# Kernel tuning notes

Measured on AMD Instinct MI355X. Metric: run time of the kernel, lower is better.

Reference implementation:

```python
import jax, jax.numpy as jnp
import numpy as np
import math

B, S, E = 2, 2048, 1024
H = 16                      # n_state_heads
STATE_SIZE = 16384
O = math.isqrt(STATE_SIZE // H)   # state_head_order = 32
C = E // (O * H)            # embedding_state_head_order_chunk_size = 2
N_BLOCKS = 12
EPS = 1e-5


def layernorm(x, g):
    mu = jnp.mean(x, axis=-1, keepdims=True)
    var = jnp.mean(jnp.square(x - mu), axis=-1, keepdims=True)
    return (x - mu) * jax.lax.rsqrt(var + EPS) * g


def setup_inputs() -> dict:
    key = jax.random.key(0)
    ks = jax.random.split(key, 8)
    return {
        "activations": jax.random.normal(ks[0], (B, S, E), dtype=jnp.float32),
        # note: torch init zeros W_up; we use small random weights so the scan is non-trivial
        "W_up": jax.random.normal(ks[1], (O, C), dtype=jnp.float32) * 0.02,
        "W_down": jax.random.normal(ks[2], (C, O), dtype=jnp.float32) * (0.02 * math.sqrt(STATE_SIZE)),
        "W_mru": jax.random.normal(ks[3], (E, E), dtype=jnp.float32) * (0.02 / math.sqrt(N_BLOCKS)),
        "g_ln1": jnp.ones((E,), dtype=jnp.float32),
        "g_ln2": jnp.ones((E,), dtype=jnp.float32),
        "W_mlp1": jax.random.normal(ks[4], (4 * E, E), dtype=jnp.float32) * 0.02,
        "W_mlp2": jax.random.normal(ks[5], (E, 4 * E), dtype=jnp.float32) * (0.02 / math.sqrt(N_BLOCKS)),
    }


def reference(activations, W_up, W_down, W_mru, g_ln1, g_ln2, W_mlp1, W_mlp2):
    x = activations                                   # [B,S,E]
    h = layernorm(x, g_ln1)
    hh = h.reshape(B, S, H, O, C)                     # unflatten(-1, (H, O, C))
    # state_matrices_up (Linear C->O, no bias) + eye  -> per-token transition matrices
    M = jnp.einsum('bshoc,qc->bshoq', hh, W_up) + jnp.eye(O, dtype=h.dtype)  # [B,S,H,O,O]
    Mt = jnp.swapaxes(M, 1, 2)                        # [B,H,S,O,O]
    # cumulative non-commutative matrix products along the sequence (log-depth scan)
    P = jax.lax.associative_scan(jnp.matmul, Mt, axis=2)  # P[t] = M_0 @ ... @ M_t
    states = jnp.swapaxes(P, 1, 2)                    # [B,S,H,O,O]
    # state_matrices_down (Linear O->C, no bias), then flatten(-3,-1)
    down = jnp.einsum('bshoq,cq->bshoc', states, W_down).reshape(B, S, E)
    mru_out = down @ W_mru.T
    x = x + mru_out
    y = layernorm(x, g_ln2)
    m = jax.nn.gelu(y @ W_mlp1.T, approximate=False) @ W_mlp2.T
    x = x + m
    new_state = states[-1]                            # faithful to torch states[-1] (last batch element): [S,H,O,O]
    return (x, new_state)
```

## Files before the change

### kernel.cpp

```cpp
#include <hip/hip_runtime.h>
#include <hip/hip_bf16.h>
#include <math.h>

#define Bb 2
#define Ss 2048
#define Ee 1024
#define Hh 16
#define Oo 32
#define Cc 2
#define EPSf 1e-5f
#define NSEG 64
#define SEGL 32
#define NGRP 8
#define GRPL 8

typedef __hip_bfloat16 bf16;
typedef __attribute__((ext_vector_type(8))) short short8;
typedef __attribute__((ext_vector_type(4))) float f32x4;

template <typename OT>
__global__ __launch_bounds__(256) void ln_kernel(const float* __restrict__ x,
                                                 const float* __restrict__ g,
                                                 OT* __restrict__ out) {
    __shared__ float red[8];
    int row = blockIdx.x;
    const float4* xr = (const float4*)(x + (size_t)row * Ee);
    float4 v = xr[threadIdx.x];
    float s = v.x + v.y + v.z + v.w;
#pragma unroll
    for (int off = 32; off > 0; off >>= 1) s += __shfl_xor(s, off);
    int wave = threadIdx.x >> 6, lane = threadIdx.x & 63;
    if (!lane) red[wave] = s;
    __syncthreads();
    float mu = (red[0] + red[1] + red[2] + red[3]) * (1.0f / Ee);
    float dx = v.x - mu, dy = v.y - mu, dz = v.z - mu, dw = v.w - mu;
    float sq = dx * dx + dy * dy + dz * dz + dw * dw;
#pragma unroll
    for (int off = 32; off > 0; off >>= 1) sq += __shfl_xor(sq, off);
    if (!lane) red[wave + 4] = sq;
    __syncthreads();
    float var = (red[4] + red[5] + red[6] + red[7]) * (1.0f / Ee);
    float rs = rsqrtf(var + EPSf);
    float4 gv = ((const float4*)g)[threadIdx.x];
    float o0 = dx * rs * gv.x, o1 = dy * rs * gv.y, o2 = dz * rs * gv.z, o3 = dw * rs * gv.w;
    if constexpr (sizeof(OT) == 4) {
        ((float4*)((float*)out + (size_t)row * Ee))[threadIdx.x] = make_float4(o0, o1, o2, o3);
    } else {
        __align__(8) bf16 t[4] = {__float2bfloat16(o0), __float2bfloat16(o1),
                                  __float2bfloat16(o2), __float2bfloat16(o3)};
        ((ushort4*)((unsigned short*)out + (size_t)row * Ee))[threadIdx.x] = *(const ushort4*)t;
    }
}

__device__ __forceinline__ void cvt4(const float* in, bf16* out, int i) {
    float4 v = ((const float4*)in)[i];
    __align__(8) bf16 t[4] = {__float2bfloat16(v.x), __float2bfloat16(v.y),
                              __float2bfloat16(v.z), __float2bfloat16(v.w)};
    ((ushort4*)out)[i] = *(const ushort4*)t;
}

__global__ __launch_bounds__(256) void f2bf3_kernel(const float* __restrict__ a, bf16* __restrict__ oa,
                                                    const float* __restrict__ b, bf16* __restrict__ ob,
                                                    const float* __restrict__ c, bf16* __restrict__ oc) {
    const int nA = (1024 * 1024) / 4;
    const int nB = (4 * 1024 * 1024) / 4;
    int i = blockIdx.x * 256 + threadIdx.x;
    if (i < nA) cvt4(a, oa, i);
    else if (i < nA + nB) cvt4(b, ob, i - nA);
    else cvt4(c, oc, i - nA - nB);
}

__device__ __forceinline__ void row_matmul(float e[32], const float* __restrict__ T) {
    float r[32];
#pragma unroll
    for (int q = 0; q < 32; ++q) r[q] = 0.f;
#pragma unroll
    for (int kk = 0; kk < 32; ++kk) {
        float ekk = e[kk];
        const float4* tr = (const float4*)(T + kk * 32);
#pragma unroll
        for (int j = 0; j < 8; ++j) {
            float4 tv = tr[j];
            r[4 * j + 0] = fmaf(ekk, tv.x, r[4 * j + 0]);
            r[4 * j + 1] = fmaf(ekk, tv.y, r[4 * j + 1]);
            r[4 * j + 2] = fmaf(ekk, tv.z, r[4 * j + 2]);
            r[4 * j + 3] = fmaf(ekk, tv.w, r[4 * j + 3]);
        }
    }
#pragma unroll
    for (int q = 0; q < 32; ++q) e[q] = r[q];
}

__global__ __launch_bounds__(256, 2) void scan_pass1(const float* __restrict__ h,
                                                     const float* __restrict__ Wup,
                                                     float* __restrict__ Ttot) {
    int wv = __builtin_amdgcn_readfirstlane((int)(threadIdx.x >> 6));
    int lane = threadIdx.x & 63;
    int o = lane & 31;
    int seg = blockIdx.x * 4 + wv;
    int chain = seg >> 6;
    int g = seg & 63;
    int b = chain >> 4, head = chain & 15;

    float wq[64];
#pragma unroll
    for (int j = 0; j < 16; ++j) ((float4*)wq)[j] = ((const float4*)Wup)[j];
    float p[32];
#pragma unroll
    for (int q = 0; q < 32; ++q) p[q] = (q == o) ? 1.0f : 0.0f;

    const float* hb = h + ((size_t)b * Ss + (size_t)g * SEGL) * Ee + head * 64;
    float4 ac[16];
#pragma unroll
    for (int j = 0; j < 16; ++j) ac[j] = ((const float4*)hb)[j];

    for (int st = 0; st < SEGL; ++st) {
        float4 an[16];
        if (st + 1 < SEGL) {
            const float4* hn = (const float4*)(hb + (size_t)(st + 1) * Ee);
#pragma unroll
            for (int j = 0; j < 16; ++j) an[j] = hn[j];
        }
        float s0 = 0.f, s1 = 0.f, u0 = 0.f, u1 = 0.f;
#pragma unroll
        for (int q = 0; q < 32; q += 2) {
            float4 v = ac[q >> 1];
            s0 = fmaf(p[q], v.x, s0);
            u0 = fmaf(p[q], v.y, u0);
            s1 = fmaf(p[q + 1], v.z, s1);
            u1 = fmaf(p[q + 1], v.w, u1);
        }
        float y0 = s0 + s1, y1 = u0 + u1;
#pragma unroll
        for (int q = 0; q < 32; ++q) p[q] = fmaf(y0, wq[2 * q], fmaf(y1, wq[2 * q + 1], p[q]));
        if (st + 1 < SEGL) {
#pragma unroll
            for (int j = 0; j < 16; ++j) ac[j] = an[j];
        }
    }
    if (lane < 32) {
        float* tb = Ttot + ((size_t)chain * NSEG + g) * 1024 + o * 32;
#pragma unroll
        for (int j = 0; j < 8; ++j)
            ((float4*)tb)[j] = make_float4(p[4 * j], p[4 * j + 1], p[4 * j + 2], p[4 * j + 3]);
    }
}

__global__ __launch_bounds__(64) void scan_pass2a(const float* __restrict__ Ttot,
                                                  float* __restrict__ Eexc,
                                                  float* __restrict__ Utot) {
    int lane = threadIdx.x & 63;
    int o = lane & 31;
    int grp = blockIdx.x;
    int chain = grp >> 3, k = grp & 7;
    float e[32];
#pragma unroll
    for (int q = 0; q < 32; ++q) e[q] = (q == o) ? 1.0f : 0.0f;
    for (int i = 0; i < GRPL; ++i) {
        int g = k * GRPL + i;
        if (lane < 32) {
            float* eb = Eexc + ((size_t)chain * NSEG + g) * 1024 + o * 32;
#pragma unroll
            for (int j = 0; j < 8; ++j)
                ((float4*)eb)[j] = make_float4(e[4 * j], e[4 * j + 1], e[4 * j + 2], e[4 * j + 3]);
        }
        row_matmul(e, Ttot + ((size_t)chain * NSEG + g) * 1024);
    }
    if (lane < 32) {
        float* ub = Utot + ((size_t)chain * NGRP + k) * 1024 + o * 32;
#pragma unroll
        for (int j = 0; j < 8; ++j)
            ((float4*)ub)[j] = make_float4(e[4 * j], e[4 * j + 1], e[4 * j + 2], e[4 * j + 3]);
    }
}

__global__ __launch_bounds__(64) void scan_pass2b(const float* __restrict__ Utot,
                                                  float* __restrict__ Wkp) {
    int lane = threadIdx.x & 63;
    int o = lane & 31;
    int chain = blockIdx.x;
    float w[32];
#pragma unroll
    for (int q = 0; q < 32; ++q) w[q] = (q == o) ? 1.0f : 0.0f;
    for (int k = 0; k < NGRP; ++k) {
        if (lane < 32) {
            float* wb = Wkp + ((size_t)chain * NGRP + k) * 1024 + o * 32;
#pragma unroll
            for (int j = 0; j < 8; ++j)
                ((float4*)wb)[j] = make_float4(w[4 * j], w[4 * j + 1], w[4 * j + 2], w[4 * j + 3]);
        }
        row_matmul(w, Utot + ((size_t)chain * NGRP + k) * 1024);
    }
}

__global__ __launch_bounds__(256, 2) void scan_pass3(const float* __restrict__ h,
                                                     const float* __restrict__ Wup,
                                                     const float* __restrict__ Wdn,
                                                     const float* __restrict__ Eexc,
                                                     const float* __restrict__ Wkp,
                                                     bf16* __restrict__ down,
                                                     float* __restrict__ state_out) {
    int wv = __builtin_amdgcn_readfirstlane((int)(threadIdx.x >> 6));
    int lane = threadIdx.x & 63;
    int o = lane & 31;
    int seg = blockIdx.x * 4 + wv;
    int chain = seg >> 6;
    int g = seg & 63;
    int b = chain >> 4, head = chain & 15;
    int k = g >> 3;

    float wq[64];
#pragma unroll
    for (int j = 0; j < 16; ++j) ((float4*)wq)[j] = ((const float4*)Wup)[j];
    float wd[64];
#pragma unroll
    for (int j = 0; j < 16; ++j) ((float4*)wd)[j] = ((const float4*)Wdn)[j];

    float G00 = 0.f, G01 = 0.f, G10 = 0.f, G11 = 0.f;
#pragma unroll
    for (int q = 0; q < 32; ++q) {
        G00 = fmaf(wq[2 * q + 0], wd[q], G00);
        G01 = fmaf(wq[2 * q + 0], wd[32 + q], G01);
        G10 = fmaf(wq[2 * q + 1], wd[q], G10);
        G11 = fmaf(wq[2 * q + 1], wd[32 + q], G11);
    }

    float wrow[32];
    const float* wb = Wkp + ((size_t)chain * NGRP + k) * 1024 + o * 32;
#pragma unroll
    for (int j = 0; j < 8; ++j) ((float4*)wrow)[j] = ((const float4*)wb)[j];
    const float* Eb = Eexc + ((size_t)chain * NSEG + g) * 1024;
    float p[32];
#pragma unroll
    for (int q = 0; q < 32; ++q) p[q] = 0.f;
#pragma unroll
    for (int kk = 0; kk < 32; ++kk) {
        float wkk = wrow[kk];
        const float4* er = (const float4*)(Eb + kk * 32);
#pragma unroll
        for (int j = 0; j < 8; ++j) {
            float4 ev = er[j];
            p[4 * j + 0] = fmaf(wkk, ev.x, p[4 * j + 0]);
            p[4 * j + 1] = fmaf(wkk, ev.y, p[4 * j + 1]);
            p[4 * j + 2] = fmaf(wkk, ev.z, p[4 * j + 2]);
            p[4 * j + 3] = fmaf(wkk, ev.w, p[4 * j + 3]);
        }
    }

    float d0 = 0.f, d1 = 0.f;
#pragma unroll
    for (int q = 0; q < 32; ++q) {
        d0 = fmaf(p[q], wd[q], d0);
        d1 = fmaf(p[q], wd[32 + q], d1);
    }

    const float* hb = h + ((size_t)b * Ss + (size_t)g * SEGL) * Ee + head * 64;
    bf16* db = down + ((size_t)b * Ss + (size_t)g * SEGL) * Ee + head * 64 + o * 2;
    float* sb = state_out + ((size_t)g * SEGL * Hh + head) * 1024 + o * 32;

    float4 ac[16];
#pragma unroll
    for (int j = 0; j < 16; ++j) ac[j] = ((const float4*)hb)[j];

    for (int st = 0; st < SEGL; ++st) {
        float4 an[16];
        if (st + 1 < SEGL) {
            const float4* hn = (const float4*)(hb + (size_t)(st + 1) * Ee);
#pragma unroll
            for (int j = 0; j < 16; ++j) an[j] = hn[j];
        }
        float s0 = 0.f, s1 = 0.f, u0 = 0.f, u1 = 0.f;
#pragma unroll
        for (int q = 0; q < 32; q += 2) {
            float4 v = ac[q >> 1];
            s0 = fmaf(p[q], v.x, s0);
            u0 = fmaf(p[q], v.y, u0);
            s1 = fmaf(p[q + 1], v.z, s1);
            u1 = fmaf(p[q + 1], v.w, u1);
        }
        float y0 = s0 + s1, y1 = u0 + u1;
#pragma unroll
        for (int q = 0; q < 32; ++q) p[q] = fmaf(y0, wq[2 * q], fmaf(y1, wq[2 * q + 1], p[q]));
        d0 = fmaf(y0, G00, fmaf(y1, G10, d0));
        d1 = fmaf(y0, G01, fmaf(y1, G11, d1));
        if (lane < 32) {
            __hip_bfloat162 dv;
            dv.x = __float2bfloat16(d0);
            dv.y = __float2bfloat16(d1);
            *(__hip_bfloat162*)(db + (size_t)st * Ee) = dv;
            if (b == Bb - 1) {
                float* sp = sb + (size_t)st * (Hh * 1024);
#pragma unroll
                for (int j = 0; j < 8; ++j)
                    ((float4*)sp)[j] = make_float4(p[4 * j], p[4 * j + 1], p[4 * j + 2], p[4 * j + 3]);
            }
        }
        if (st + 1 < SEGL) {
#pragma unroll
            for (int j = 0; j < 16; ++j) ac[j] = an[j];
        }
    }
}

__device__ __forceinline__ void load_lds16(const bf16* g, short* l) {
    __builtin_amdgcn_global_load_lds((const __attribute__((address_space(1))) unsigned int*)g,
                                     (__attribute__((address_space(3))) unsigned int*)l,
                                     16, 0, 0);
}


template <bool GELU, bool RESID, bool BF16OUT>
__global__ __launch_bounds__(256, 2) void mgemm64(const bf16* __restrict__ A,
                                                  const bf16* __restrict__ Wt,
                                                  const float* __restrict__ res,
                                                  float* __restrict__ Cf,
                                                  bf16* __restrict__ Cb,
                                                  int M, int N, int K) {
    __shared__ __align__(16) short As[3][64 * 32];
    __shared__ __align__(16) short Bs[3][128 * 32];
    int tid = threadIdx.x;
    int w = __builtin_amdgcn_readfirstlane(tid >> 6);
    int l = tid & 63;

    int nbm = M >> 6, nbn = N >> 7;
    int nwg = nbm * nbn;
    int cpx = nwg >> 3;
    int v = ((int)blockIdx.x & 7) * cpx + ((int)blockIdx.x >> 3);
    int sq = v >> 6, rem = v & 63;
    int sqPerRow = nbn >> 3;
    int bm = (sq / sqPerRow) * 8 + (rem >> 3);
    int bn = (sq % sqPerRow) * 8 + (rem & 7);

    int wr = w >> 1, wc = w & 1;
    int lr = l & 15;
    int lks = (((l >> 4) ^ ((lr >> 1) & 3)) * 8);

    int srow = tid >> 2;
    int scol = ((tid & 3) ^ ((tid >> 3) & 3)) * 8;
    const bf16* ga  = A + (size_t)(bm * 64 + srow) * K + scol;
    const bf16* gb0 = Wt + (size_t)(bn * 128 + srow) * K + scol;
    const bf16* gb1 = Wt + (size_t)(bn * 128 + 64 + srow) * K + scol;

    f32x4 acc[2][4];
#pragma unroll
    for (int m = 0; m < 2; ++m)
#pragma unroll
        for (int n = 0; n < 4; ++n) acc[m][n] = (f32x4){0.f, 0.f, 0.f, 0.f};

#define STAGE64(d, kt)                                       \
    do {                                                     \
        int _off = (kt) * 32;                                \
        load_lds16(ga + _off, &As[d][w * 512]);              \
        load_lds16(gb0 + _off, &Bs[d][w * 512]);             \
        load_lds16(gb1 + _off, &Bs[d][2048 + w * 512]);      \
    } while (0)

    const int NK = K >> 5;
    STAGE64(0, 0);
    STAGE64(1, 1);
    STAGE64(2, 2);
    asm volatile("s_waitcnt vmcnt(6)" ::: "memory");
    __builtin_amdgcn_sched_barrier(0);
    __builtin_amdgcn_s_barrier();

    for (int t = 0; t < NK; ++t) {
        int d = t % 3;
        short8 af[2], bfr[4];
#pragma unroll
        for (int m = 0; m < 2; ++m)
            af[m] = *(const short8*)&As[d][(wr * 32 + m * 16 + lr) * 32 + lks];
#pragma unroll
        for (int n = 0; n < 4; ++n)
            bfr[n] = *(const short8*)&Bs[d][(wc * 64 + n * 16 + lr) * 32 + lks];
        asm volatile("s_waitcnt lgkmcnt(0)" ::: "memory");
        __builtin_amdgcn_sched_barrier(0);
        __builtin_amdgcn_s_barrier();
        if (t + 3 < NK) STAGE64(d, t + 3);
        __builtin_amdgcn_sched_barrier(0);
        __builtin_amdgcn_s_setprio(1);
#pragma unroll
        for (int m = 0; m < 2; ++m)
#pragma unroll
            for (int n = 0; n < 4; ++n)
                acc[m][n] = __builtin_amdgcn_mfma_f32_16x16x32_bf16(af[m], bfr[n], acc[m][n], 0, 0, 0);
        __builtin_amdgcn_s_setprio(0);
        if (t + 3 < NK) {
            asm volatile("s_waitcnt vmcnt(6)" ::: "memory");
        } else if (t + 2 < NK) {
            asm volatile("s_waitcnt vmcnt(3)" ::: "memory");
        } else if (t + 1 < NK) {
            asm volatile("s_waitcnt vmcnt(0)" ::: "memory");
        }
        __builtin_amdgcn_sched_barrier(0);
        __builtin_amdgcn_s_barrier();
    }
#undef STAGE64

#pragma unroll
    for (int m = 0; m < 2; ++m) {
#pragma unroll
        for (int n = 0; n < 4; ++n) {
            int gr0 = bm * 64 + wr * 32 + m * 16 + (l >> 4) * 4;
            int gc = bn * 128 + wc * 64 + n * 16 + lr;
#pragma unroll
            for (int j = 0; j < 4; ++j) {
                float v2 = acc[m][n][j];
                if (GELU) v2 = 0.5f * v2 * (1.0f + erff(v2 * 0.70710678118654752f));
                if (RESID) v2 += res[(size_t)(gr0 + j) * N + gc];
                if (BF16OUT) Cb[(size_t)(gr0 + j) * N + gc] = __float2bfloat16(v2);
                else Cf[(size_t)(gr0 + j) * N + gc] = v2;
            }
        }
    }
}

__global__ __launch_bounds__(512, 2) void mgemm8(const bf16* __restrict__ A,
                                                 const bf16* __restrict__ Wt,
                                                 bf16* __restrict__ Cb,
                                                 int M, int N, int K) {
    __shared__ __align__(16) short As[3][256 * 32];
    __shared__ __align__(16) short Bs[3][256 * 32];
    int tid = threadIdx.x;
    int w = __builtin_amdgcn_readfirstlane(tid >> 6);
    int l = tid & 63;

    int nbm = M >> 8, nbn = N >> 8;
    int nwg = nbm * nbn;
    int cpx = nwg >> 3;
    int v = ((int)blockIdx.x & 7) * cpx + ((int)blockIdx.x >> 3);
    int sq = v >> 6, rem = v & 63;
    int sqPerRow = nbn >> 3;
    int bm = (sq / sqPerRow) * 8 + (rem >> 3);
    int bn = (sq % sqPerRow) * 8 + (rem & 7);

    int wr = w >> 2, wc = w & 3;
    int lr = l & 15;
    int lks = (((l >> 4) ^ ((lr >> 1) & 3)) * 8);

    int srow = tid >> 2;
    int scol = ((tid & 3) ^ ((tid >> 3) & 3)) * 8;
    const bf16* ga0 = A + (size_t)(bm * 256 + srow) * K + scol;
    const bf16* ga1 = A + (size_t)(bm * 256 + 128 + srow) * K + scol;
    const bf16* gb0 = Wt + (size_t)(bn * 256 + srow) * K + scol;
    const bf16* gb1 = Wt + (size_t)(bn * 256 + 128 + srow) * K + scol;

    f32x4 acc[8][4];
#pragma unroll
    for (int m = 0; m < 8; ++m)
#pragma unroll
        for (int n = 0; n < 4; ++n) acc[m][n] = (f32x4){0.f, 0.f, 0.f, 0.f};

#define STAGE8(d, kt)                                        \
    do {                                                     \
        int _off = (kt) * 32;                                \
        load_lds16(ga0 + _off, &As[d][w * 512]);             \
        load_lds16(ga1 + _off, &As[d][4096 + w * 512]);      \
        load_lds16(gb0 + _off, &Bs[d][w * 512]);             \
        load_lds16(gb1 + _off, &Bs[d][4096 + w * 512]);      \
    } while (0)

    const int NK = K >> 5;
    STAGE8(0, 0);
    STAGE8(1, 1);
    STAGE8(2, 2);
    asm volatile("s_waitcnt vmcnt(8)" ::: "memory");
    __builtin_amdgcn_sched_barrier(0);
    __builtin_amdgcn_s_barrier();

    for (int t = 0; t < NK; ++t) {
        int d = t % 3;
        short8 af[8], bfr[4];
#pragma unroll
        for (int m = 0; m < 8; ++m)
            af[m] = *(const short8*)&As[d][(wr * 128 + m * 16 + lr) * 32 + lks];
#pragma unroll
        for (int n = 0; n < 4; ++n)
            bfr[n] = *(const short8*)&Bs[d][(wc * 64 + n * 16 + lr) * 32 + lks];
        asm volatile("s_waitcnt lgkmcnt(0)" ::: "memory");
        __builtin_amdgcn_sched_barrier(0);
        __builtin_amdgcn_s_barrier();
        if (t + 3 < NK) STAGE8(d, t + 3);
        __builtin_amdgcn_sched_barrier(0);
        __builtin_amdgcn_s_setprio(1);
#pragma unroll
        for (int m = 0; m < 8; ++m)
#pragma unroll
            for (int n = 0; n < 4; ++n)
                acc[m][n] = __builtin_amdgcn_mfma_f32_16x16x32_bf16(af[m], bfr[n], acc[m][n], 0, 0, 0);
        __builtin_amdgcn_s_setprio(0);
        if (t + 3 < NK) {
            asm volatile("s_waitcnt vmcnt(8)" ::: "memory");
        } else if (t + 2 < NK) {
            asm volatile("s_waitcnt vmcnt(4)" ::: "memory");
        } else if (t + 1 < NK) {
            asm volatile("s_waitcnt vmcnt(0)" ::: "memory");
        }
        __builtin_amdgcn_sched_barrier(0);
        __builtin_amdgcn_s_barrier();
    }
#undef STAGE8

#pragma unroll
    for (int m = 0; m < 8; ++m) {
#pragma unroll
        for (int n = 0; n < 4; ++n) {
            int gr0 = bm * 256 + wr * 128 + m * 16 + (l >> 4) * 4;
            int gc = bn * 256 + wc * 64 + n * 16 + lr;
#pragma unroll
            for (int j = 0; j < 4; ++j) {
                float vv = acc[m][n][j];
                vv = 0.5f * vv * (1.0f + erff(vv * 0.70710678118654752f));
                Cb[(size_t)(gr0 + j) * N + gc] = __float2bfloat16(vv);
            }
        }
    }
}

extern "C" void kernel_launch(void* const* d_in, const int* in_sizes, int n_in,
                              void* d_out, int out_size, void* d_ws, size_t ws_size,
                              hipStream_t stream) {
    const float* act    = (const float*)d_in[0];
    const float* W_up   = (const float*)d_in[1];
    const float* W_down = (const float*)d_in[2];
    const float* W_mru  = (const float*)d_in[3];
    const float* g_ln1  = (const float*)d_in[4];
    const float* g_ln2  = (const float*)d_in[5];
    const float* W_mlp1 = (const float*)d_in[6];
    const float* W_mlp2 = (const float*)d_in[7];

    float* out_x     = (float*)d_out;
    float* out_state = (float*)d_out + (size_t)Bb * Ss * Ee;

    float* wsf = (float*)d_ws;
    const size_t Mfl = 1024 * 1024;
    float* h        = wsf;
    bf16*  down_bf  = (bf16*)(wsf + 4 * Mfl);
    bf16*  y_bf     = (bf16*)(wsf + 6 * Mfl);
    bf16*  t1_bf    = (bf16*)(wsf + 8 * Mfl);
    float* Ttot = wsf + 8 * Mfl;
    float* Eexc = wsf + 10 * Mfl;
    float* Utot = wsf + 12 * Mfl;
    float* Wkp  = wsf + 12 * Mfl + 512 * 1024;
    bf16*  Wmru_bf  = (bf16*)(wsf + 16 * Mfl);
    bf16*  Wmlp1_bf = (bf16*)(wsf + 17 * Mfl);
    bf16*  Wmlp2_bf = (bf16*)(wsf + 19 * Mfl);

    const int MT = Bb * Ss;

    f2bf3_kernel<<<9216, 256, 0, stream>>>(W_mru, Wmru_bf, W_mlp1, Wmlp1_bf, W_mlp2, Wmlp2_bf);

    ln_kernel<float><<<MT, 256, 0, stream>>>(act, g_ln1, h);
    scan_pass1<<<512, 256, 0, stream>>>(h, W_up, Ttot);
    scan_pass2a<<<256, 64, 0, stream>>>(Ttot, Eexc, Utot);
    scan_pass2b<<<32, 64, 0, stream>>>(Utot, Wkp);
    scan_pass3<<<512, 256, 0, stream>>>(h, W_up, W_down, Eexc, Wkp, down_bf, out_state);

    {
        mgemm64<false, true, false><<<(MT / 64) * (Ee / 128), 256, 0, stream>>>(
            down_bf, Wmru_bf, act, out_x, nullptr, MT, Ee, Ee);
    }
    ln_kernel<bf16><<<MT, 256, 0, stream>>>(out_x, g_ln2, y_bf);
    {
        mgemm8<<<(MT / 256) * (4 * Ee / 256), 512, 0, stream>>>(
            y_bf, Wmlp1_bf, t1_bf, MT, 4 * Ee, Ee);
    }
    {
        mgemm64<false, true, false><<<(MT / 64) * (Ee / 128), 256, 0, stream>>>(
            t1_bf, Wmlp2_bf, out_x, out_x, nullptr, MT, Ee, 4 * Ee);
    }
}
```

Before: 403.7 us.

## Fuse LN1 with weight conversion, use head-major h layout, merge scan pass2 kernels

The first layernorm and the bf16 weight conversion now run in a single prep kernel, and the normalized output is written in a head-major [B,H,S,64] layout. Each scan wave then reads contiguous 256-byte rows instead of rows strided by the embedding width. The two small pass-2 kernels become one 512-thread block per chain that keeps the group products in LDS and computes the group prefixes inside that block. This removes two launches and a global round-trip for Utot. In exchange, each wave in the merged pass2 recomputes up to seven matrix products serially, which adds some redundant work.

```diff
diff --git a/kernel.cpp b/kernel.cpp
--- a/kernel.cpp
+++ b/kernel.cpp
@@ -59,15 +59,48 @@
     ((ushort4*)out)[i] = *(const ushort4*)t;
 }
 
-__global__ __launch_bounds__(256) void f2bf3_kernel(const float* __restrict__ a, bf16* __restrict__ oa,
-                                                    const float* __restrict__ b, bf16* __restrict__ ob,
-                                                    const float* __restrict__ c, bf16* __restrict__ oc) {
-    const int nA = (1024 * 1024) / 4;
-    const int nB = (4 * 1024 * 1024) / 4;
-    int i = blockIdx.x * 256 + threadIdx.x;
-    if (i < nA) cvt4(a, oa, i);
-    else if (i < nA + nB) cvt4(b, ob, i - nA);
-    else cvt4(c, oc, i - nA - nB);
+__global__ __launch_bounds__(256) void prep_kernel(const float* __restrict__ act,
+                                                   const float* __restrict__ g,
+                                                   float* __restrict__ hs,
+                                                   const float* __restrict__ wa, bf16* __restrict__ oa,
+                                                   const float* __restrict__ wb, bf16* __restrict__ ob,
+                                                   const float* __restrict__ wc, bf16* __restrict__ oc) {
+    int bid = blockIdx.x;
+    if (bid < Bb * Ss) {
+        __shared__ float red[8];
+        int row = bid;
+        const float4* xr = (const float4*)(act + (size_t)row * Ee);
+        float4 v = xr[threadIdx.x];
+        float s = v.x + v.y + v.z + v.w;
+#pragma unroll
+        for (int off = 32; off > 0; off >>= 1) s += __shfl_xor(s, off);
+        int wave = threadIdx.x >> 6, lane = threadIdx.x & 63;
+        if (!lane) red[wave] = s;
+        __syncthreads();
+        float mu = (red[0] + red[1] + red[2] + red[3]) * (1.0f / Ee);
+        float dx = v.x - mu, dy = v.y - mu, dz = v.z - mu, dw = v.w - mu;
+        float sq = dx * dx + dy * dy + dz * dz + dw * dw;
+#pragma unroll
+        for (int off = 32; off > 0; off >>= 1) sq += __shfl_xor(sq, off);
+        if (!lane) red[wave + 4] = sq;
+        __syncthreads();
+        float var = (red[4] + red[5] + red[6] + red[7]) * (1.0f / Ee);
+        float rs = rsqrtf(var + EPSf);
+        float4 gv = ((const float4*)g)[threadIdx.x];
+        float o0 = dx * rs * gv.x, o1 = dy * rs * gv.y, o2 = dz * rs * gv.z, o3 = dw * rs * gv.w;
+        int b = row >> 11, t = row & 2047;
+        int e0 = threadIdx.x * 4;
+        int head = e0 >> 6;
+        float* dst = hs + (((size_t)(b * Hh + head) * Ss) + t) * 64 + (e0 & 63);
+        *(float4*)dst = make_float4(o0, o1, o2, o3);
+    } else {
+        int i = (bid - Bb * Ss) * 256 + threadIdx.x;
+        const int nA = (1024 * 1024) / 4;
+        const int nB = (4 * 1024 * 1024) / 4;
+        if (i < nA) cvt4(wa, oa, i);
+        else if (i < nA + nB) cvt4(wb, ob, i - nA);
+        else cvt4(wc, oc, i - nA - nB);
+    }
 }
 
 __device__ __forceinline__ void row_matmul(float e[32], const float* __restrict__ T) {
@@ -91,7 +124,7 @@
     for (int q = 0; q < 32; ++q) e[q] = r[q];
 }
 
-__global__ __launch_bounds__(256, 2) void scan_pass1(const float* __restrict__ h,
+__global__ __launch_bounds__(256, 2) void scan_pass1(const float* __restrict__ hs,
                                                      const float* __restrict__ Wup,
                                                      float* __restrict__ Ttot) {
     int wv = __builtin_amdgcn_readfirstlane((int)(threadIdx.x >> 6));
@@ -100,7 +133,6 @@
     int seg = blockIdx.x * 4 + wv;
     int chain = seg >> 6;
     int g = seg & 63;
-    int b = chain >> 4, head = chain & 15;
 
     float wq[64];
 #pragma unroll
@@ -109,7 +141,7 @@
 #pragma unroll
     for (int q = 0; q < 32; ++q) p[q] = (q == o) ? 1.0f : 0.0f;
 
-    const float* hb = h + ((size_t)b * Ss + (size_t)g * SEGL) * Ee + head * 64;
+    const float* hb = hs + ((size_t)chain * Ss + (size_t)g * SEGL) * 64;
     float4 ac[16];
 #pragma unroll
     for (int j = 0; j < 16; ++j) ac[j] = ((const float4*)hb)[j];
@@ -117,7 +149,7 @@
     for (int st = 0; st < SEGL; ++st) {
         float4 an[16];
         if (st + 1 < SEGL) {
-            const float4* hn = (const float4*)(hb + (size_t)(st + 1) * Ee);
+            const float4* hn = (const float4*)(hb + (size_t)(st + 1) * 64);
 #pragma unroll
             for (int j = 0; j < 16; ++j) an[j] = hn[j];
         }
@@ -146,13 +178,15 @@
     }
 }
 
-__global__ __launch_bounds__(64) void scan_pass2a(const float* __restrict__ Ttot,
+__global__ __launch_bounds__(512) void scan_pass2(const float* __restrict__ Ttot,
                                                   float* __restrict__ Eexc,
-                                                  float* __restrict__ Utot) {
+                                                  float* __restrict__ Wkp) {
+    __shared__ float Ush[8][1024];
+    int chain = blockIdx.x;
+    int k = __builtin_amdgcn_readfirstlane((int)(threadIdx.x >> 6));
     int lane = threadIdx.x & 63;
     int o = lane & 31;
-    int grp = blockIdx.x;
-    int chain = grp >> 3, k = grp & 7;
+
     float e[32];
 #pragma unroll
     for (int q = 0; q < 32; ++q) e[q] = (q == o) ? 1.0f : 0.0f;
@@ -167,33 +201,25 @@
         row_matmul(e, Ttot + ((size_t)chain * NSEG + g) * 1024);
     }
     if (lane < 32) {
-        float* ub = Utot + ((size_t)chain * NGRP + k) * 1024 + o * 32;
+        float* ub = &Ush[k][o * 32];
 #pragma unroll
         for (int j = 0; j < 8; ++j)
             ((float4*)ub)[j] = make_float4(e[4 * j], e[4 * j + 1], e[4 * j + 2], e[4 * j + 3]);
     }
-}
-
-__global__ __launch_bounds__(64) void scan_pass2b(const float* __restrict__ Utot,
-                                                  float* __restrict__ Wkp) {
-    int lane = threadIdx.x & 63;
-    int o = lane & 31;
-    int chain = blockIdx.x;
-    float w[32];
-#pragma unroll
-    for (int q = 0; q < 32; ++q) w[q] = (q == o) ? 1.0f : 0.0f;
-    for (int k = 0; k < NGRP; ++k) {
-        if (lane < 32) {
-            float* wb = Wkp + ((size_t)chain * NGRP + k) * 1024 + o * 32;
-#pragma unroll
-            for (int j = 0; j < 8; ++j)
-                ((float4*)wb)[j] = make_float4(w[4 * j], w[4 * j + 1], w[4 * j + 2], w[4 * j + 3]);
-        }
-        row_matmul(w, Utot + ((size_t)chain * NGRP + k) * 1024);
-    }
-}
-
-__global__ __launch_bounds__(256, 2) void scan_pass3(const float* __restrict__ h,
+    __syncthreads();
+    float wreg[32];
+#pragma unroll
+    for (int q = 0; q < 32; ++q) wreg[q] = (q == o) ? 1.0f : 0.0f;
+    for (int j = 0; j < k; ++j) row_matmul(wreg, &Ush[j][0]);
+    if (lane < 32) {
+        float* wb = Wkp + ((size_t)chain * NGRP + k) * 1024 + o * 32;
+#pragma unroll
+        for (int j = 0; j < 8; ++j)
+            ((float4*)wb)[j] = make_float4(wreg[4 * j], wreg[4 * j + 1], wreg[4 * j + 2], wreg[4 * j + 3]);
+    }
+}
+
+__global__ __launch_bounds__(256, 2) void scan_pass3(const float* __restrict__ hs,
                                                      const float* __restrict__ Wup,
                                                      const float* __restrict__ Wdn,
                                                      const float* __restrict__ Eexc,
@@ -254,7 +280,7 @@
         d1 = fmaf(p[q], wd[32 + q], d1);
     }
 
-    const float* hb = h + ((size_t)b * Ss + (size_t)g * SEGL) * Ee + head * 64;
+    const float* hb = hs + ((size_t)chain * Ss + (size_t)g * SEGL) * 64;
     bf16* db = down + ((size_t)b * Ss + (size_t)g * SEGL) * Ee + head * 64 + o * 2;
     float* sb = state_out + ((size_t)g * SEGL * Hh + head) * 1024 + o * 32;
 
@@ -265,7 +291,7 @@
     for (int st = 0; st < SEGL; ++st) {
         float4 an[16];
         if (st + 1 < SEGL) {
-            const float4* hn = (const float4*)(hb + (size_t)(st + 1) * Ee);
+            const float4* hn = (const float4*)(hb + (size_t)(st + 1) * 64);
 #pragma unroll
             for (int j = 0; j < 16; ++j) an[j] = hn[j];
         }
@@ -307,7 +333,6 @@
                                      (__attribute__((address_space(3))) unsigned int*)l,
                                      16, 0, 0);
 }
-
 
 template <bool GELU, bool RESID, bool BF16OUT>
 __global__ __launch_bounds__(256, 2) void mgemm64(const bf16* __restrict__ A,
@@ -533,39 +558,29 @@
 
     float* wsf = (float*)d_ws;
     const size_t Mfl = 1024 * 1024;
-    float* h        = wsf;
+    float* hs       = wsf;
     bf16*  down_bf  = (bf16*)(wsf + 4 * Mfl);
     bf16*  y_bf     = (bf16*)(wsf + 6 * Mfl);
     bf16*  t1_bf    = (bf16*)(wsf + 8 * Mfl);
     float* Ttot = wsf + 8 * Mfl;
     float* Eexc = wsf + 10 * Mfl;
-    float* Utot = wsf + 12 * Mfl;
-    float* Wkp  = wsf + 12 * Mfl + 512 * 1024;
+    float* Wkp  = wsf + 12 * Mfl;
     bf16*  Wmru_bf  = (bf16*)(wsf + 16 * Mfl);
     bf16*  Wmlp1_bf = (bf16*)(wsf + 17 * Mfl);
     bf16*  Wmlp2_bf = (bf16*)(wsf + 19 * Mfl);
 
     const int MT = Bb * Ss;
 
-    f2bf3_kernel<<<9216, 256, 0, stream>>>(W_mru, Wmru_bf, W_mlp1, Wmlp1_bf, W_mlp2, Wmlp2_bf);
-
-    ln_kernel<float><<<MT, 256, 0, stream>>>(act, g_ln1, h);
-    scan_pass1<<<512, 256, 0, stream>>>(h, W_up, Ttot);
-    scan_pass2a<<<256, 64, 0, stream>>>(Ttot, Eexc, Utot);
-    scan_pass2b<<<32, 64, 0, stream>>>(Utot, Wkp);
-    scan_pass3<<<512, 256, 0, stream>>>(h, W_up, W_down, Eexc, Wkp, down_bf, out_state);
-
-    {
-        mgemm64<false, true, false><<<(MT / 64) * (Ee / 128), 256, 0, stream>>>(
-            down_bf, Wmru_bf, act, out_x, nullptr, MT, Ee, Ee);
-    }
+    prep_kernel<<<MT + 9216, 256, 0, stream>>>(act, g_ln1, hs,
+                                               W_mru, Wmru_bf, W_mlp1, Wmlp1_bf, W_mlp2, Wmlp2_bf);
+    scan_pass1<<<512, 256, 0, stream>>>(hs, W_up, Ttot);
+    scan_pass2<<<32, 512, 0, stream>>>(Ttot, Eexc, Wkp);
+    scan_pass3<<<512, 256, 0, stream>>>(hs, W_up, W_down, Eexc, Wkp, down_bf, out_state);
+    mgemm64<false, true, false><<<(MT / 64) * (Ee / 128), 256, 0, stream>>>(
+        down_bf, Wmru_bf, act, out_x, nullptr, MT, Ee, Ee);
     ln_kernel<bf16><<<MT, 256, 0, stream>>>(out_x, g_ln2, y_bf);
-    {
-        mgemm8<<<(MT / 256) * (4 * Ee / 256), 512, 0, stream>>>(
-            y_bf, Wmlp1_bf, t1_bf, MT, 4 * Ee, Ee);
-    }
-    {
-        mgemm64<false, true, false><<<(MT / 64) * (Ee / 128), 256, 0, stream>>>(
-            t1_bf, Wmlp2_bf, out_x, out_x, nullptr, MT, Ee, 4 * Ee);
-    }
-}
+    mgemm8<<<(MT / 256) * (4 * Ee / 256), 512, 0, stream>>>(
+        y_bf, Wmlp1_bf, t1_bf, MT, 4 * Ee, Ee);
+    mgemm64<false, true, false><<<(MT / 64) * (Ee / 128), 256, 0, stream>>>(
+        t1_bf, Wmlp2_bf, out_x, out_x, nullptr, MT, Ee, 4 * Ee);
+}
```

Measured after the change: 339.7 us. 1.19x faster.
